# Performance work log

Measured on AMD Instinct MI355X. Metric: run time of the kernel, lower is better.

## Reference

```python
import jax, jax.numpy as jnp
import numpy as np

LEVEL = 8
THRESHOLD = 0.1
INV_SQRT2 = 0.7071067811865476  # 1/sqrt(2), db1 (Haar) filter coefficient

# Static frequency-order permutation: pywt get_level(order='freq') places the
# natural-order (path-lex: aa,ad,da,dd,...) node n at frequency position gray(n).
_g = np.arange(2 ** LEVEL)
_FREQ_PERM = np.argsort(_g ^ (_g >> 1))  # freq[j] = natural[_FREQ_PERM[j]]


def setup_inputs() -> dict:
    key = jax.random.key(0)
    x = jax.random.normal(key, (128, 65536), dtype=jnp.float32)
    return {"x": x}


def _wavelet_packet_leaves(x):
    """Full db1 wavelet-packet tree to LEVEL; returns [B, 2^L, T/2^L] in freq order.

    For Haar with even-length inputs, pywt's symmetric extension is a no-op:
    a[k] = (x[2k]+x[2k+1])/sqrt2, d[k] = (x[2k]-x[2k+1])/sqrt2.
    """
    B, T = x.shape
    c = x[:, None, :]  # [B, nodes=1, len=T]
    for _ in range(LEVEL):
        ev = c[..., 0::2]
        od = c[..., 1::2]
        a = (ev + od) * INV_SQRT2
        d = (ev - od) * INV_SQRT2
        # interleave children (a,d) adjacent -> natural (path-lex) node order
        c = jnp.concatenate([a[:, :, None, :], d[:, :, None, :]], axis=2)
        c = c.reshape(B, -1, a.shape[-1])
    return c[:, _FREQ_PERM, :]


def reference(x):
    coeffs = _wavelet_packet_leaves(x)          # [B, 2^L, n]
    p = coeffs * coeffs
    p = p / (jnp.sum(p, axis=-1, keepdims=True) + 1e-8)
    entropy = -jnp.sum(p * jnp.log(p + 1e-8), axis=-1)  # [B, 2^L]
    keep = entropy > THRESHOLD                           # [B, 2^L] bool
    # Original returns per-batch stacks of kept nodes (variable length);
    # jit-friendly equivalent: zero out pruned nodes and return the mask.
    out = jnp.where(keep[..., None], coeffs, jnp.zeros((), coeffs.dtype))
    return out, entropy, keep
```

## Files before the change

kernel.cpp:

```cpp
#include <hip/hip_runtime.h>

static constexpr int BROWS = 128;
static constexpr int T     = 65536;
static constexpr int CL    = 256;
static constexpr int NCH   = 256;
static constexpr int NODES = 256;
static constexpr int KG    = 32;
static constexpr int NPH   = NCH / KG;
static constexpr int LSTR  = 257;
static constexpr int NTHR  = 512;

__device__ __forceinline__ int freq_pos(int h) {
    unsigned r = __brev((unsigned)h) >> 24;
    return (int)(r ^ (r >> 1));
}

__device__ __forceinline__ void bfly01(float4& v) {
    float4 w;
    w.x = v.x + v.y; w.y = v.x - v.y;
    w.z = v.z + v.w; w.w = v.z - v.w;
    v.x = w.x + w.z; v.z = w.x - w.z;
    v.y = w.y + w.w; v.w = w.y - w.w;
}

template<int CTRL>
__device__ __forceinline__ float xchg_dpp(float v) {
    return __builtin_bit_cast(float,
        __builtin_amdgcn_update_dpp(0, __builtin_bit_cast(int, v), CTRL, 0xF, 0xF, true));
}

template<int CTRL>
__device__ __forceinline__ void stage_dpp(float4& v1, float4& v2, float sgn) {
    float o;
    o = xchg_dpp<CTRL>(v1.x); v1.x = fmaf(sgn, v1.x, o);
    o = xchg_dpp<CTRL>(v1.y); v1.y = fmaf(sgn, v1.y, o);
    o = xchg_dpp<CTRL>(v1.z); v1.z = fmaf(sgn, v1.z, o);
    o = xchg_dpp<CTRL>(v1.w); v1.w = fmaf(sgn, v1.w, o);
    o = xchg_dpp<CTRL>(v2.x); v2.x = fmaf(sgn, v2.x, o);
    o = xchg_dpp<CTRL>(v2.y); v2.y = fmaf(sgn, v2.y, o);
    o = xchg_dpp<CTRL>(v2.z); v2.z = fmaf(sgn, v2.z, o);
    o = xchg_dpp<CTRL>(v2.w); v2.w = fmaf(sgn, v2.w, o);
}

__device__ __forceinline__ void stage_shfl(float4& v1, float4& v2, float sgn, int mask) {
    float o;
    o = __shfl_xor(v1.x, mask, 64); v1.x = fmaf(sgn, v1.x, o);
    o = __shfl_xor(v1.y, mask, 64); v1.y = fmaf(sgn, v1.y, o);
    o = __shfl_xor(v1.z, mask, 64); v1.z = fmaf(sgn, v1.z, o);
    o = __shfl_xor(v1.w, mask, 64); v1.w = fmaf(sgn, v1.w, o);
    o = __shfl_xor(v2.x, mask, 64); v2.x = fmaf(sgn, v2.x, o);
    o = __shfl_xor(v2.y, mask, 64); v2.y = fmaf(sgn, v2.y, o);
    o = __shfl_xor(v2.z, mask, 64); v2.z = fmaf(sgn, v2.z, o);
    o = __shfl_xor(v2.w, mask, 64); v2.w = fmaf(sgn, v2.w, o);
}

__global__ __launch_bounds__(NTHR) void wht_row(const float* __restrict__ x,
                                                float* __restrict__ coeffs,
                                                float* __restrict__ entropy,
                                                float* __restrict__ keep) {
    __shared__ float lds[KG][LSTR];

    const int b    = blockIdx.x;
    const int lane = threadIdx.x & 63;
    const int wave = threadIdx.x >> 6;
    const int half = lane >> 5;
    const int L    = lane & 31;

    const float* xb = x + (size_t)b * T;

    int npos1[4], npos2[4];
    #pragma unroll
    for (int i = 0; i < 4; ++i) {
        npos1[i] = freq_pos(4 * L + i);
        npos2[i] = freq_pos(128 + 4 * L + i);
    }
    float A1[4] = {0.f,0.f,0.f,0.f}, B1[4] = {0.f,0.f,0.f,0.f};
    float A2[4] = {0.f,0.f,0.f,0.f}, B2[4] = {0.f,0.f,0.f,0.f};

    const float sgn0 = 1.0f - 2.0f * (float)((L >> 0) & 1);
    const float sgn1 = 1.0f - 2.0f * (float)((L >> 1) & 1);
    const float sgn2 = 1.0f - 2.0f * (float)((L >> 2) & 1);
    const float sgn3 = 1.0f - 2.0f * (float)((L >> 3) & 1);
    const float sgn4 = 1.0f - 2.0f * (float)((L >> 4) & 1);

    const int kl0 = wave * 4 + half;
    const int kl1 = wave * 4 + 2 + half;
    const int col = 4 * L;

    float4 c0a = *(const float4*)(xb + (size_t)kl0 * CL + col);
    float4 c0b = *(const float4*)(xb + (size_t)kl0 * CL + col + 128);
    float4 c1a = *(const float4*)(xb + (size_t)kl1 * CL + col);
    float4 c1b = *(const float4*)(xb + (size_t)kl1 * CL + col + 128);

    #pragma unroll
    for (int ph = 0; ph < NPH; ++ph) {
        float4 n0a, n0b, n1a, n1b;
        if (ph + 1 < NPH) {
            const float* q0 = xb + (size_t)((ph + 1) * KG + kl0) * CL + col;
            const float* q1 = xb + (size_t)((ph + 1) * KG + kl1) * CL + col;
            n0a = *(const float4*)(q0);
            n0b = *(const float4*)(q0 + 128);
            n1a = *(const float4*)(q1);
            n1b = *(const float4*)(q1 + 128);
        }

        #pragma unroll
        for (int it = 0; it < 2; ++it) {
            const int kl = (it == 0) ? kl0 : kl1;
            float4 v1 = (it == 0) ? c0a : c1a;
            float4 v2 = (it == 0) ? c0b : c1b;

            float4 t;
            t.x = v1.x - v2.x; t.y = v1.y - v2.y; t.z = v1.z - v2.z; t.w = v1.w - v2.w;
            v1.x += v2.x; v1.y += v2.y; v1.z += v2.z; v1.w += v2.w;
            v2 = t;

            bfly01(v1);
            bfly01(v2);

            stage_dpp<0xB1>(v1, v2, sgn0);
            stage_dpp<0x4E>(v1, v2, sgn1);
            stage_shfl(v1, v2, sgn2, 4);
            stage_dpp<0x128>(v1, v2, sgn3);
            stage_shfl(v1, v2, sgn4, 16);

            float c1r[4] = {v1.x*0.0625f, v1.y*0.0625f, v1.z*0.0625f, v1.w*0.0625f};
            float c2r[4] = {v2.x*0.0625f, v2.y*0.0625f, v2.z*0.0625f, v2.w*0.0625f};
            #pragma unroll
            for (int i = 0; i < 4; ++i) {
                const float s1 = c1r[i] * c1r[i];
                A1[i] += s1;
                B1[i] += s1 * __logf(s1 + 1e-35f);
                lds[kl][npos1[i]] = c1r[i];
                const float s2 = c2r[i] * c2r[i];
                A2[i] += s2;
                B2[i] += s2 * __logf(s2 + 1e-35f);
                lds[kl][npos2[i]] = c2r[i];
            }
        }
        __syncthreads();

        float* ob = coeffs + (size_t)b * T + ph * KG;
        const int kk = (threadIdx.x & 7) * 4;
        const int m0 = threadIdx.x >> 3;
        #pragma unroll
        for (int p = 0; p < 4; ++p) {
            const int m = p * 64 + m0;
            float4 v;
            v.x = lds[kk + 0][m];
            v.y = lds[kk + 1][m];
            v.z = lds[kk + 2][m];
            v.w = lds[kk + 3][m];
            *(float4*)(ob + (size_t)m * NCH + kk) = v;
        }
        __syncthreads();

        c0a = n0a; c0b = n0b; c1a = n1a; c1b = n1b;
    }

    #pragma unroll
    for (int i = 0; i < 4; ++i) {
        A1[i] += __shfl_xor(A1[i], 32, 64); B1[i] += __shfl_xor(B1[i], 32, 64);
        A2[i] += __shfl_xor(A2[i], 32, 64); B2[i] += __shfl_xor(B2[i], 32, 64);
    }
    float* pl = &lds[0][0];
    if (half == 0) {
        #pragma unroll
        for (int i = 0; i < 4; ++i) {
            pl[wave * 512 + npos1[i]]       = A1[i];
            pl[wave * 512 + 256 + npos1[i]] = B1[i];
            pl[wave * 512 + npos2[i]]       = A2[i];
            pl[wave * 512 + 256 + npos2[i]] = B2[i];
        }
    }
    __syncthreads();

    const int idx = threadIdx.x;
    float s = 0.f;
    #pragma unroll
    for (int w = 0; w < 8; ++w) s += pl[w * 512 + idx];
    pl[idx] = s;
    __syncthreads();

    if (idx < NODES) {
        const float A = pl[idx];
        const float B = pl[256 + idx];
        const float S = A + 1e-8f;
        const float e = (A * __logf(S) - B) / S;
        const bool kp = e > 0.1f;

        entropy[b * NODES + idx] = e;
        keep[b * NODES + idx]    = kp ? 1.0f : 0.0f;

        if (!kp) {
            float4 z = make_float4(0.f, 0.f, 0.f, 0.f);
            float4* cp = (float4*)(coeffs + ((size_t)b * NODES + idx) * NCH);
            for (int j = 0; j < NCH / 4; ++j) cp[j] = z;
        }
    }
}

extern "C" void kernel_launch(void* const* d_in, const int* in_sizes, int n_in,
                              void* d_out, int out_size, void* d_ws, size_t ws_size,
                              hipStream_t stream) {
    const float* x = (const float*)d_in[0];

    float* coeffs  = (float*)d_out;
    float* entropy = coeffs + (size_t)BROWS * NODES * NCH;
    float* keepf   = entropy + (size_t)BROWS * NODES;

    (void)d_ws; (void)ws_size;

    wht_row<<<dim3(BROWS), dim3(NTHR), 0, stream>>>(x, coeffs, entropy, keepf);
}
```

Measured before the change: 91.17 us.

## Double workgroup size and double-buffer LDS transpose to drop a barrier

Raises the workgroup from 512 to 1024 threads, so each wave transforms one 256-sample chunk per phase instead of two. The LDS transpose buffer is now double-buffered, which removes the second __syncthreads per phase. The final per-node reduction is widened to 16 waves. The aim is more waves in flight per CU to hide memory latency, since only 128 blocks run on the device. The cost is twice the LDS per block and more register pressure under the 1024-thread launch bound.

Measured after the change: 94.61 us. +3.8%, slower.

```diff
diff --git a/kernel.cpp b/kernel.cpp
--- a/kernel.cpp
+++ b/kernel.cpp
@@ -8,7 +8,7 @@
 static constexpr int KG    = 32;
 static constexpr int NPH   = NCH / KG;
 static constexpr int LSTR  = 257;
-static constexpr int NTHR  = 512;
+static constexpr int NTHR  = 1024;
 
 __device__ __forceinline__ int freq_pos(int h) {
     unsigned r = __brev((unsigned)h) >> 24;
@@ -54,15 +54,16 @@
     o = __shfl_xor(v2.w, mask, 64); v2.w = fmaf(sgn, v2.w, o);
 }
 
-__global__ __launch_bounds__(NTHR) void wht_row(const float* __restrict__ x,
-                                                float* __restrict__ coeffs,
-                                                float* __restrict__ entropy,
-                                                float* __restrict__ keep) {
-    __shared__ float lds[KG][LSTR];
+__global__ __launch_bounds__(NTHR, 4) void wht_row(const float* __restrict__ x,
+                                                   float* __restrict__ coeffs,
+                                                   float* __restrict__ entropy,
+                                                   float* __restrict__ keep) {
+    __shared__ float lds[2][KG][LSTR];
 
     const int b    = blockIdx.x;
-    const int lane = threadIdx.x & 63;
-    const int wave = threadIdx.x >> 6;
+    const int tid  = threadIdx.x;
+    const int lane = tid & 63;
+    const int wave = tid >> 6;
     const int half = lane >> 5;
     const int L    = lane & 31;
 
@@ -83,79 +84,71 @@
     const float sgn3 = 1.0f - 2.0f * (float)((L >> 3) & 1);
     const float sgn4 = 1.0f - 2.0f * (float)((L >> 4) & 1);
 
-    const int kl0 = wave * 4 + half;
-    const int kl1 = wave * 4 + 2 + half;
+    const int kl  = wave * 2 + half;
     const int col = 4 * L;
 
-    float4 c0a = *(const float4*)(xb + (size_t)kl0 * CL + col);
-    float4 c0b = *(const float4*)(xb + (size_t)kl0 * CL + col + 128);
-    float4 c1a = *(const float4*)(xb + (size_t)kl1 * CL + col);
-    float4 c1b = *(const float4*)(xb + (size_t)kl1 * CL + col + 128);
+    float4 va = *(const float4*)(xb + (size_t)kl * CL + col);
+    float4 vb = *(const float4*)(xb + (size_t)kl * CL + col + 128);
+
+    const int kk = (tid & 7) * 4;
+    const int m0 = tid >> 3;
 
     #pragma unroll
     for (int ph = 0; ph < NPH; ++ph) {
-        float4 n0a, n0b, n1a, n1b;
+        const int buf = ph & 1;
+
+        float4 na, nb;
         if (ph + 1 < NPH) {
-            const float* q0 = xb + (size_t)((ph + 1) * KG + kl0) * CL + col;
-            const float* q1 = xb + (size_t)((ph + 1) * KG + kl1) * CL + col;
-            n0a = *(const float4*)(q0);
-            n0b = *(const float4*)(q0 + 128);
-            n1a = *(const float4*)(q1);
-            n1b = *(const float4*)(q1 + 128);
-        }
-
-        #pragma unroll
-        for (int it = 0; it < 2; ++it) {
-            const int kl = (it == 0) ? kl0 : kl1;
-            float4 v1 = (it == 0) ? c0a : c1a;
-            float4 v2 = (it == 0) ? c0b : c1b;
-
-            float4 t;
-            t.x = v1.x - v2.x; t.y = v1.y - v2.y; t.z = v1.z - v2.z; t.w = v1.w - v2.w;
-            v1.x += v2.x; v1.y += v2.y; v1.z += v2.z; v1.w += v2.w;
-            v2 = t;
-
-            bfly01(v1);
-            bfly01(v2);
-
-            stage_dpp<0xB1>(v1, v2, sgn0);
-            stage_dpp<0x4E>(v1, v2, sgn1);
-            stage_shfl(v1, v2, sgn2, 4);
-            stage_dpp<0x128>(v1, v2, sgn3);
-            stage_shfl(v1, v2, sgn4, 16);
-
-            float c1r[4] = {v1.x*0.0625f, v1.y*0.0625f, v1.z*0.0625f, v1.w*0.0625f};
-            float c2r[4] = {v2.x*0.0625f, v2.y*0.0625f, v2.z*0.0625f, v2.w*0.0625f};
-            #pragma unroll
-            for (int i = 0; i < 4; ++i) {
-                const float s1 = c1r[i] * c1r[i];
-                A1[i] += s1;
-                B1[i] += s1 * __logf(s1 + 1e-35f);
-                lds[kl][npos1[i]] = c1r[i];
-                const float s2 = c2r[i] * c2r[i];
-                A2[i] += s2;
-                B2[i] += s2 * __logf(s2 + 1e-35f);
-                lds[kl][npos2[i]] = c2r[i];
-            }
-        }
+            const float* q = xb + (size_t)((ph + 1) * KG + kl) * CL + col;
+            na = *(const float4*)(q);
+            nb = *(const float4*)(q + 128);
+        }
+
+        float4 v1 = va, v2 = vb;
+
+        float4 t;
+        t.x = v1.x - v2.x; t.y = v1.y - v2.y; t.z = v1.z - v2.z; t.w = v1.w - v2.w;
+        v1.x += v2.x; v1.y += v2.y; v1.z += v2.z; v1.w += v2.w;
+        v2 = t;
+
+        bfly01(v1);
+        bfly01(v2);
+
+        stage_dpp<0xB1>(v1, v2, sgn0);
+        stage_dpp<0x4E>(v1, v2, sgn1);
+        stage_shfl(v1, v2, sgn2, 4);
+        stage_dpp<0x128>(v1, v2, sgn3);
+        stage_shfl(v1, v2, sgn4, 16);
+
+        float c1r[4] = {v1.x*0.0625f, v1.y*0.0625f, v1.z*0.0625f, v1.w*0.0625f};
+        float c2r[4] = {v2.x*0.0625f, v2.y*0.0625f, v2.z*0.0625f, v2.w*0.0625f};
+        #pragma unroll
+        for (int i = 0; i < 4; ++i) {
+            const float s1 = c1r[i] * c1r[i];
+            A1[i] += s1;
+            B1[i] += s1 * __logf(s1 + 1e-35f);
+            lds[buf][kl][npos1[i]] = c1r[i];
+            const float s2 = c2r[i] * c2r[i];
+            A2[i] += s2;
+            B2[i] += s2 * __logf(s2 + 1e-35f);
+            lds[buf][kl][npos2[i]] = c2r[i];
+        }
+
         __syncthreads();
 
         float* ob = coeffs + (size_t)b * T + ph * KG;
-        const int kk = (threadIdx.x & 7) * 4;
-        const int m0 = threadIdx.x >> 3;
-        #pragma unroll
-        for (int p = 0; p < 4; ++p) {
-            const int m = p * 64 + m0;
+        #pragma unroll
+        for (int p = 0; p < 2; ++p) {
+            const int m = p * 128 + m0;
             float4 v;
-            v.x = lds[kk + 0][m];
-            v.y = lds[kk + 1][m];
-            v.z = lds[kk + 2][m];
-            v.w = lds[kk + 3][m];
+            v.x = lds[buf][kk + 0][m];
+            v.y = lds[buf][kk + 1][m];
+            v.z = lds[buf][kk + 2][m];
+            v.w = lds[buf][kk + 3][m];
             *(float4*)(ob + (size_t)m * NCH + kk) = v;
         }
-        __syncthreads();
-
-        c0a = n0a; c0b = n0b; c1a = n1a; c1b = n1b;
+
+        va = na; vb = nb;
     }
 
     #pragma unroll
@@ -163,7 +156,7 @@
         A1[i] += __shfl_xor(A1[i], 32, 64); B1[i] += __shfl_xor(B1[i], 32, 64);
         A2[i] += __shfl_xor(A2[i], 32, 64); B2[i] += __shfl_xor(B2[i], 32, 64);
     }
-    float* pl = &lds[0][0];
+    float* pl = &lds[0][0][0];
     if (half == 0) {
         #pragma unroll
         for (int i = 0; i < 4; ++i) {
@@ -175,26 +168,27 @@
     }
     __syncthreads();
 
-    const int idx = threadIdx.x;
-    float s = 0.f;
-    #pragma unroll
-    for (int w = 0; w < 8; ++w) s += pl[w * 512 + idx];
-    pl[idx] = s;
+    if (tid < 512) {
+        float s = 0.f;
+        #pragma unroll
+        for (int w = 0; w < 16; ++w) s += pl[w * 512 + tid];
+        pl[tid] = s;
+    }
     __syncthreads();
 
-    if (idx < NODES) {
-        const float A = pl[idx];
-        const float B = pl[256 + idx];
+    if (tid < NODES) {
+        const float A = pl[tid];
+        const float B = pl[256 + tid];
         const float S = A + 1e-8f;
         const float e = (A * __logf(S) - B) / S;
         const bool kp = e > 0.1f;
 
-        entropy[b * NODES + idx] = e;
-        keep[b * NODES + idx]    = kp ? 1.0f : 0.0f;
+        entropy[b * NODES + tid] = e;
+        keep[b * NODES + tid]    = kp ? 1.0f : 0.0f;
 
         if (!kp) {
             float4 z = make_float4(0.f, 0.f, 0.f, 0.f);
-            float4* cp = (float4*)(coeffs + ((size_t)b * NODES + idx) * NCH);
+            float4* cp = (float4*)(coeffs + ((size_t)b * NODES + tid) * NCH);
             for (int j = 0; j < NCH / 4; ++j) cp[j] = z;
         }
     }
```
